# Optimization experiments

Hardware: AMD Instinct MI355X
Metric: run time of the kernel (lower is better)

The kernel has to match this reference:

```python
import jax, jax.numpy as jnp
import numpy as np

B_, S_, DM, DI, N_, R_, K_ = 2, 2048, 256, 512, 16, 32, 4
NB = 4  # 2 forward + 2 backward MambaBlocks


def setup_inputs() -> dict:
    key = jax.random.key(0)
    ks = jax.random.split(key, 16)
    def rn(k, shape, s=0.02):
        return jax.random.normal(k, shape, jnp.float32) * s
    A = jnp.log(jnp.arange(1, N_ + 1, dtype=jnp.float32))  # [N]
    return {
        'x': jax.random.normal(ks[0], (B_, S_, DM), jnp.float32),
        'in_w': rn(ks[1], (NB, DM, 2 * DI)),
        'conv_w': rn(ks[2], (NB, DI, K_), 0.3),
        'conv_b': jnp.zeros((NB, DI), jnp.float32),
        'A_log': jnp.broadcast_to(A, (NB, DI, N_)) + 0.0,
        'xd_w': rn(ks[3], (NB, DI, R_)),
        'xB_w': rn(ks[4], (NB, DI, N_)),
        'xC_w': rn(ks[5], (NB, DI, N_)),
        'dtp_w': rn(ks[6], (NB, R_, DI), R_ ** -0.5),
        'dtp_b': jax.random.uniform(ks[7], (NB, DI), jnp.float32,
                                    minval=jnp.log(0.001), maxval=jnp.log(0.1)),
        'D': jnp.ones((NB, DI), jnp.float32),
        'out_w': rn(ks[8], (NB, DI, DM)),
        'ln_g': jnp.ones((NB, DM), jnp.float32),
        'ln_b': jnp.zeros((NB, DM), jnp.float32),
        'merge_w': rn(ks[9], (2 * DM, DM)),
    }


def _layer_norm(x, g, b, eps=1e-5):
    m = jnp.mean(x, axis=-1, keepdims=True)
    v = jnp.mean(jnp.square(x - m), axis=-1, keepdims=True)
    return (x - m) * jax.lax.rsqrt(v + eps) * g + b


def _ssm_scan(dA, dBx, C):
    # dA, dBx: [B,S,DI,N]; C: [B,S,N] -> y: [B,S,DI]
    def step(h, inp):
        dA_t, dBx_t, C_t = inp
        h = dA_t * h + dBx_t                      # [B,DI,N]
        y = jnp.einsum('bdn,bn->bd', h, C_t)      # [B,DI]
        return h, y
    h0 = jnp.zeros(dA.shape[:1] + dA.shape[2:], dA.dtype)
    _, ys = jax.lax.scan(step, h0, (dA.transpose(1, 0, 2, 3),
                                    dBx.transpose(1, 0, 2, 3),
                                    C.transpose(1, 0, 2)))
    return ys.transpose(1, 0, 2)


def _mamba_block(x, in_w, conv_w, conv_b, A_log, xd_w, xB_w, xC_w,
                 dtp_w, dtp_b, D, out_w, g, b):
    res = x
    xn = _layer_norm(x, g, b)
    xz = xn @ in_w                                # [B,S,2*DI]
    xs, z = jnp.split(xz, 2, axis=-1)
    # causal depthwise conv: left pad K-1 (equals torch pad=K-1 then slice [:S])
    xc = jax.lax.conv_general_dilated(
        xs.transpose(0, 2, 1), conv_w[:, None, :], (1,), [(K_ - 1, 0)],
        dimension_numbers=('NCH', 'OIH', 'NCH'), feature_group_count=DI)
    xc = jax.nn.silu((xc + conv_b[None, :, None]).transpose(0, 2, 1))  # [B,S,DI]
    delta = jax.nn.softplus((xc @ xd_w) @ dtp_w + dtp_b)               # [B,S,DI]
    Bm = xc @ xB_w                                # [B,S,N]
    Cm = xc @ xC_w                                # [B,S,N]
    A = -jnp.exp(A_log)                           # [DI,N]
    dA = jnp.exp(delta[..., None] * A)            # [B,S,DI,N]
    dBx = (delta * xc)[..., None] * Bm[:, :, None, :]
    y = _ssm_scan(dA, dBx, Cm) + D * xc
    return (y * jax.nn.silu(z)) @ out_w + res


def reference(x, in_w, conv_w, conv_b, A_log, xd_w, xB_w, xC_w,
              dtp_w, dtp_b, D, out_w, ln_g, ln_b, merge_w):
    def blk(h, i):
        return _mamba_block(h, in_w[i], conv_w[i], conv_b[i], A_log[i],
                            xd_w[i], xB_w[i], xC_w[i], dtp_w[i], dtp_b[i],
                            D[i], out_w[i], ln_g[i], ln_b[i])
    fwd = blk(blk(x, 0), 1)
    bwd = blk(blk(x[:, ::-1], 2), 3)[:, ::-1]
    return jnp.concatenate([fwd, bwd], axis=-1) @ merge_w
```

## Files before the change

kernel.cpp:

```cpp
#include <hip/hip_runtime.h>

#define S_LEN 2048
#define DINNER 512
#define NCHUNK 64
#define CLEN 32

typedef unsigned short u16;
typedef short bf16x8 __attribute__((ext_vector_type(8)));
typedef unsigned short u16x8 __attribute__((ext_vector_type(8)));
typedef float f32x4 __attribute__((ext_vector_type(4)));

__device__ __forceinline__ float bf2f(u16 u) {
  unsigned int x = ((unsigned int)u) << 16;
  float f; __builtin_memcpy(&f, &x, 4); return f;
}
__device__ __forceinline__ u16 f2bf(float f) {
  unsigned int x; __builtin_memcpy(&x, &f, 4);
  return (u16)((x + 0x7FFFu + ((x >> 16) & 1u)) >> 16);
}
__device__ __forceinline__ float ldw(const void* p, size_t i, int isbf) {
  return isbf ? bf2f(((const u16*)p)[i]) : ((const float*)p)[i];
}
__device__ __forceinline__ float siluf(float x) { return x / (1.f + __expf(-x)); }
__device__ __forceinline__ float softplusf(float x) {
  if (x > 20.f) return x;
  return log1pf(__expf(x));
}

__global__ __launch_bounds__(256) void detect_kernel(const void* __restrict__ x,
                                                     int* __restrict__ flag) {
  __shared__ int cnt;
  if (threadIdx.x == 0) cnt = 0;
  __syncthreads();
  u16 u = ((const u16*)x)[2 * threadIdx.x];
  int e = (u >> 7) & 0xFF;
  if (e >= 0x60 && e <= 0x8F) atomicAdd(&cnt, 1);
  __syncthreads();
  if (threadIdx.x == 0) *flag = (cnt > 128) ? 1 : 0;
}

__global__ __launch_bounds__(256) void prep_kernel(
    const void* __restrict__ A_log,
    const void* __restrict__ in_w, const void* __restrict__ out_w,
    const void* __restrict__ merge_w,
    const void* __restrict__ xdw, const void* __restrict__ dtpw,
    const void* __restrict__ xBw, const void* __restrict__ xCw,
    const int* __restrict__ pf,
    float* __restrict__ Acp, u16* __restrict__ Wp_in, u16* __restrict__ Wp_out,
    u16* __restrict__ Wp_mg, u16* __restrict__ Wp_cmb)
{
  const int isbf = *pf;
  int b = blockIdx.x;
  int tid = threadIdx.x;
  __shared__ float smem[32 * 163];
  float* tile = smem;

  if (b < 128) {
    int idx = b * 256 + tid;
    Acp[idx] = -__expf(ldw(A_log, (size_t)idx, isbf));
    return;
  }
  b -= 128;

  if (b < 512 + 256 + 64) {
    const void* src; u16* dst; int K, N, nb64, kb, mat;
    if (b < 512)      { src = in_w;    dst = Wp_in;  K = 256; N = 1024;
                        nb64 = b % 16; kb = (b / 16) % 8; mat = b / 128; }
    else if (b < 768) { int c = b - 512; src = out_w; dst = Wp_out; K = 512; N = 256;
                        nb64 = c % 4; kb = (c / 4) % 16; mat = c / 64; }
    else              { int c = b - 768; src = merge_w; dst = Wp_mg; K = 512; N = 256;
                        nb64 = c % 4; kb = (c / 4) % 16; mat = 0; }
    size_t so = (size_t)mat * K * N;
    int kk = tid >> 3, nseg = (tid & 7) * 8;
#pragma unroll
    for (int j = 0; j < 8; ++j)
      tile[kk * 65 + nseg + j] =
          ldw(src, so + (size_t)(kb * 32 + kk) * N + nb64 * 64 + nseg + j, isbf);
    __syncthreads();
    int cc = tid >> 6, i0 = (tid & 63) * 8;
    int q = i0 >> 7, nn = (i0 >> 3) & 15;
    u16 outv[8];
#pragma unroll
    for (int j = 0; j < 8; ++j) outv[j] = f2bf(tile[(q * 8 + j) * 65 + cc * 16 + nn]);
    size_t doff = (size_t)mat * K * N + ((size_t)(nb64 * 4 + cc) * (K >> 5) + kb) * 512 + i0;
    *(u16x8*)(dst + doff) = *(const u16x8*)outv;
    return;
  }
  b -= 832;

  {
    int nb64 = b % 9, kb = (b / 9) % 16, mat = b / 144;
    float* xd = smem + 32 * 65;
    float* wt = smem + 32 * 98;
    if (nb64 < 8) {
      {
        int k = tid >> 3, j0 = (tid & 7) * 4;
#pragma unroll
        for (int j = 0; j < 4; ++j)
          xd[k * 33 + j0 + j] =
              ldw(xdw, (size_t)mat * 16384 + (size_t)(kb * 32 + k) * 32 + j0 + j, isbf);
        int jj = tid >> 3, n0l = (tid & 7) * 8;
#pragma unroll
        for (int n = 0; n < 8; ++n)
          wt[jj * 65 + n0l + n] =
              ldw(dtpw, (size_t)mat * 16384 + (size_t)jj * 512 + nb64 * 64 + n0l + n, isbf);
      }
      __syncthreads();
      for (int l = tid; l < 2048; l += 256) {
        int k = l >> 6, n = l & 63;
        float a = 0.f;
#pragma unroll
        for (int j = 0; j < 32; ++j) a += xd[k * 33 + j] * wt[j * 65 + n];
        tile[k * 65 + n] = a;
      }
    } else {
      for (int l = tid; l < 2048; l += 256) {
        int k = l >> 6, n = l & 63;
        int kg = kb * 32 + k;
        float v = 0.f;
        if (n < 16)      v = ldw(xBw, (size_t)mat * 8192 + (size_t)kg * 16 + n, isbf);
        else if (n < 32) v = ldw(xCw, (size_t)mat * 8192 + (size_t)kg * 16 + (n - 16), isbf);
        tile[k * 65 + n] = v;
      }
    }
    __syncthreads();
    int cc = tid >> 6, i0 = (tid & 63) * 8;
    int q = i0 >> 7, nn = (i0 >> 3) & 15;
    u16 outv[8];
#pragma unroll
    for (int j = 0; j < 8; ++j) outv[j] = f2bf(tile[(q * 8 + j) * 65 + cc * 16 + nn]);
    size_t doff = (size_t)mat * 294912 + ((size_t)(nb64 * 4 + cc) * 16 + kb) * 512 + i0;
    *(u16x8*)(Wp_cmb + doff) = *(const u16x8*)outv;
  }
}

__global__ __launch_bounds__(256) void ln_kernel(
    const void* __restrict__ x, const u16* __restrict__ obA, int it,
    const void* __restrict__ g, const void* __restrict__ bta,
    const int* __restrict__ pf, float* __restrict__ res, u16* __restrict__ xnb)
{
  const int isbf = *pf;
  int r = blockIdx.x;
  int tid = threadIdx.x;
  int chain = r >> 12, rr = r & 4095;
  int i = chain * 2 + it;
  size_t wo = (size_t)i * 256;
  float v;
  if (it == 0) {
    int b = rr >> 11, s = rr & 2047;
    int sr = chain ? (b * S_LEN + (S_LEN - 1 - s)) : rr;
    v = ldw(x, (size_t)sr * 256 + tid, isbf);
  } else {
    v = bf2f(obA[(size_t)r * 256 + tid]);
  }
  res[(size_t)r * 256 + tid] = v;
  float s1 = v, s2 = v * v;
#pragma unroll
  for (int o = 32; o > 0; o >>= 1) {
    s1 += __shfl_xor(s1, o, 64);
    s2 += __shfl_xor(s2, o, 64);
  }
  __shared__ float r1[4], r2[4];
  if ((tid & 63) == 0) { r1[tid >> 6] = s1; r2[tid >> 6] = s2; }
  __syncthreads();
  s1 = r1[0] + r1[1] + r1[2] + r1[3];
  s2 = r2[0] + r2[1] + r2[2] + r2[3];
  float mean = s1 * (1.f / 256.f);
  float var  = s2 * (1.f / 256.f) - mean * mean;
  float inv  = rsqrtf(var + 1e-5f);
  xnb[(size_t)r * 256 + tid] =
      f2bf((v - mean) * inv * ldw(g, wo + tid, isbf) + ldw(bta, wo + tid, isbf));
}

template<int OUTMODE>
__global__ __launch_bounds__(256) void gemm64(
    const u16* __restrict__ A, const u16* __restrict__ Wp, size_t woA, size_t woB, int mhalf,
    const float* __restrict__ res, void* __restrict__ Out, void* __restrict__ Out2,
    const void* __restrict__ bias, size_t boA, size_t boB,
    const int* __restrict__ pf, int N, int K, int nbx)
{
  const int isbf = *pf;
  __shared__ __align__(16) u16 Asb[2][4096];
  __shared__ __align__(16) u16 Bsb[2][4096];
  int tid = threadIdx.x;
  int gidx = blockIdx.x;
  int xcd = gidx & 7, rest = gidx >> 3;
  int nIdx = rest % nbx, mGrp = rest / nbx;
  int n0 = nIdx * 64, m0 = (xcd + (mGrp << 3)) * 64;
  size_t wo = (mhalf && m0 >= mhalf) ? woB : woA;
  int w = tid >> 6, lane = tid & 63;
  int q = lane >> 4, r = lane & 15;
  const int wm0 = (w >> 1) * 2, wn0 = (w & 1) * 2;
  const int kbs = K >> 5;
  f32x4 acc[2][2];
#pragma unroll
  for (int i = 0; i < 2; ++i)
#pragma unroll
    for (int j = 0; j < 2; ++j) acc[i][j] = (f32x4){0.f, 0.f, 0.f, 0.f};

  int sm = tid >> 2, sq = tid & 3;
  const u16* asrc = A + (size_t)(m0 + sm) * K + sq * 8;
  const int aoff = ((sm >> 4) * 4 + sq) * 128 + (sm & 15) * 8;
  int bnb = tid >> 6, binner = (tid & 63) * 8;
  const int boff = bnb * 512 + binner;
  const u16* bcol = Wp + wo + (size_t)((n0 >> 4) + bnb) * kbs * 512 + binner;

  u16x8 la0 = *(const u16x8*)(asrc);
  u16x8 la1 = *(const u16x8*)(asrc + 32);
  u16x8 lb0 = *(const u16x8*)(bcol);
  u16x8 lb1 = *(const u16x8*)(bcol + 512);

  int p = 0;
  for (int k0 = 0; k0 < K; k0 += 64, p ^= 1) {
    *(u16x8*)(Asb[p] + aoff)        = la0;
    *(u16x8*)(Asb[p] + aoff + 2048) = la1;
    *(u16x8*)(Bsb[p] + boff)        = lb0;
    *(u16x8*)(Bsb[p] + boff + 2048) = lb1;
    __syncthreads();
    if (k0 + 64 < K) {
      la0 = *(const u16x8*)(asrc + k0 + 64);
      la1 = *(const u16x8*)(asrc + k0 + 96);
      const u16* bs = bcol + (size_t)((k0 + 64) >> 5) * 512;
      lb0 = *(const u16x8*)bs;
      lb1 = *(const u16x8*)(bs + 512);
    }
#pragma unroll
    for (int ck = 0; ck < 2; ++ck) {
      const u16* Ab = Asb[p] + ck * 2048;
      const u16* Bb = Bsb[p] + ck * 2048;
      bf16x8 af[2], bfr[2];
#pragma unroll
      for (int i = 0; i < 2; ++i)
        af[i] = *(const bf16x8*)(Ab + ((wm0 + i) * 4 + q) * 128 + r * 8);
#pragma unroll
      for (int j = 0; j < 2; ++j)
        bfr[j] = *(const bf16x8*)(Bb + ((wn0 + j) * 4 + q) * 128 + r * 8);
#pragma unroll
      for (int i = 0; i < 2; ++i)
#pragma unroll
        for (int j = 0; j < 2; ++j)
          acc[i][j] = __builtin_amdgcn_mfma_f32_16x16x32_bf16(af[i], bfr[j], acc[i][j], 0, 0, 0);
    }
  }
#pragma unroll
  for (int i = 0; i < 2; ++i) {
    int rowb = m0 + (wm0 + i) * 16 + q * 4;
#pragma unroll
    for (int j = 0; j < 2; ++j) {
      int col = n0 + (wn0 + j) * 16 + r;
#pragma unroll
      for (int t = 0; t < 4; ++t) {
        int row = rowb + t;
        float v = acc[i][j][t];
        if (OUTMODE == 2 || OUTMODE == 3) { if (res) v += res[(size_t)row * N + col]; }
        if (OUTMODE == 1) {
          size_t lidx = (size_t)row * N + col;
          if (isbf) ((u16*)Out)[lidx] = f2bf(v); else ((float*)Out)[lidx] = v;
        } else if (OUTMODE == 2) {
          ((u16*)Out)[(size_t)row * N + col] = f2bf(v);
        } else if (OUTMODE == 3) {
          int orow, cofx;
          if (row < 4096) { orow = row; cofx = 0; }
          else {
            int rr = row - 4096; int bb = rr >> 11, ss = rr & 2047;
            orow = bb * S_LEN + (S_LEN - 1 - ss); cofx = 256;
          }
          ((u16*)Out)[(size_t)orow * 512 + col + cofx] = f2bf(v);
        } else if (OUTMODE == 5) {
          if (col < 512) {
            float bv = ldw(bias, ((row < 4096) ? boA : boB) + col, isbf);
            ((u16*)Out)[(size_t)row * 512 + col] = f2bf(softplusf(v + bv));
          } else if (col < 544) {
            ((float*)Out2)[(size_t)row * 32 + (col - 512)] = v;
          }
        }
      }
    }
  }
}

__global__ __launch_bounds__(256) void conv_kernel(
    const u16* __restrict__ xzb, const void* __restrict__ cw, const void* __restrict__ cb,
    int it, const int* __restrict__ pf, u16* __restrict__ xcb)
{
  const int isbf = *pf;
  int idx = blockIdx.x * 256 + threadIdx.x;
  int r = idx >> 6, dg = idx & 63;
  int d0 = dg << 3;
  int chain = r >> 12, rr = r & 4095;
  int i = chain * 2 + it;
  size_t ow = (size_t)i * 2048, ob = (size_t)i * 512;
  int s = rr & 2047;
  float acc[8];
#pragma unroll
  for (int j = 0; j < 8; ++j) acc[j] = ldw(cb, ob + d0 + j, isbf);
#pragma unroll
  for (int k = 0; k < 4; ++k) {
    int t = s - 3 + k;
    if (t >= 0) {
      u16x8 xv = *(const u16x8*)(xzb + (((size_t)(r + t - s)) << 10) + d0);
#pragma unroll
      for (int j = 0; j < 8; ++j)
        acc[j] += ldw(cw, ow + (size_t)(d0 + j) * 4 + k, isbf) * bf2f(xv[j]);
    }
  }
  u16 outv[8];
#pragma unroll
  for (int j = 0; j < 8; ++j) outv[j] = f2bf(siluf(acc[j]));
  *(u16x8*)(xcb + ((size_t)r << 9) + d0) = *(const u16x8*)outv;
}

__global__ __launch_bounds__(256) void scan_p1_kernel(
    const u16* __restrict__ xcb, const u16* __restrict__ delb, const float* __restrict__ dBC,
    const float* __restrict__ Acp, int it, const int* __restrict__ pf,
    float* __restrict__ aggA, float* __restrict__ aggB)
{
  __shared__ float sb[32][16];
  __shared__ u16 sdu[32][64];
  __shared__ u16 sxu[32][64];
  int tid = threadIdx.x;
  int di = tid >> 2, ng = tid & 3;
  int d0 = blockIdx.x << 6;
  int c = blockIdx.y, seq = blockIdx.z;
  int chain = seq >> 1, bb = seq & 1;
  int row0 = chain * 4096 + bb * S_LEN + c * CLEN;
  int i = chain * 2 + it;
  {
    int t = tid >> 3, e0 = (tid & 7) * 8;
    *(u16x8*)&sdu[t][e0] = *(const u16x8*)(delb + (size_t)(row0 + t) * 512 + d0 + e0);
    *(u16x8*)&sxu[t][e0] = *(const u16x8*)(xcb + (size_t)(row0 + t) * 512 + d0 + e0);
  }
  if (tid < 128) {
    int t = tid >> 2, e0 = (tid & 3) * 4;
    *(f32x4*)&sb[t][e0] = *(const f32x4*)(dBC + (size_t)(row0 + t) * 32 + e0);
  }
  f32x4 Ac = *(const f32x4*)(Acp + ((size_t)i * 512 + d0 + di) * 16 + ng * 4);
  __syncthreads();
  float h[4] = {0.f, 0.f, 0.f, 0.f};
  float ap[4] = {1.f, 1.f, 1.f, 1.f};
#pragma unroll 8
  for (int t = 0; t < CLEN; ++t) {
    float de = bf2f(sdu[t][di]);
    float dx = de * bf2f(sxu[t][di]);
    f32x4 B = *(const f32x4*)&sb[t][ng * 4];
#pragma unroll
    for (int j = 0; j < 4; ++j) {
      float e = __expf(de * Ac[j]);
      h[j] = e * h[j] + dx * B[j];
      ap[j] *= e;
    }
  }
  size_t o = (((size_t)(seq * NCHUNK + c) * DINNER) + d0 + di) * 16 + ng * 4;
  *(f32x4*)(aggA + o) = (f32x4){ap[0], ap[1], ap[2], ap[3]};
  *(f32x4*)(aggB + o) = (f32x4){h[0], h[1], h[2], h[3]};
}

__global__ __launch_bounds__(64) void scan_prefix_kernel(
    const float* __restrict__ aggA, float* __restrict__ aggB)
{
  int idx = blockIdx.x * 64 + threadIdx.x;
  int n = idx & 15, d = (idx >> 4) & 511, seq = idx >> 13;
  size_t o = (((size_t)(seq * NCHUNK) * DINNER) + d) * 16 + n;
  const size_t stride = (size_t)DINNER * 16;
  float h = 0.f;
  for (int c0 = 0; c0 < NCHUNK; c0 += 8) {
    float a[8], b[8];
#pragma unroll
    for (int j = 0; j < 8; ++j) {
      a[j] = aggA[o + (size_t)j * stride];
      b[j] = aggB[o + (size_t)j * stride];
    }
#pragma unroll
    for (int j = 0; j < 8; ++j) {
      aggB[o + (size_t)j * stride] = h;
      h = a[j] * h + b[j];
    }
    o += (size_t)8 * stride;
  }
}

__global__ __launch_bounds__(256) void scan_p3_kernel(
    const u16* __restrict__ xcb, const u16* __restrict__ delb, const float* __restrict__ dBC,
    const u16* __restrict__ xzb, const float* __restrict__ hpref,
    const float* __restrict__ Acp, const void* __restrict__ Dp,
    int it, const int* __restrict__ pf, u16* __restrict__ ymb)
{
  const int isbf = *pf;
  __shared__ float sbc[32][32];
  __shared__ float sy[32][64];
  __shared__ u16 sdu[32][64];
  __shared__ u16 sxu[32][64];
  __shared__ u16 szu[32][64];
  int tid = threadIdx.x;
  int di = tid >> 2, ng = tid & 3;
  int d0 = blockIdx.x << 6;
  int c = blockIdx.y, seq = blockIdx.z;
  int chain = seq >> 1, bb = seq & 1;
  int row0 = chain * 4096 + bb * S_LEN + c * CLEN;
  int i = chain * 2 + it;
  size_t oD = (size_t)i * 512;
  {
    int t = tid >> 3, e0 = (tid & 7) * 8;
    *(u16x8*)&sdu[t][e0] = *(const u16x8*)(delb + (size_t)(row0 + t) * 512 + d0 + e0);
    *(u16x8*)&sxu[t][e0] = *(const u16x8*)(xcb + (size_t)(row0 + t) * 512 + d0 + e0);
    *(u16x8*)&szu[t][e0] = *(const u16x8*)(xzb + ((size_t)(row0 + t) << 10) + 512 + d0 + e0);
  }
  {
    int t = tid >> 3, e0 = (tid & 7) * 4;
    *(f32x4*)&sbc[t][e0] = *(const f32x4*)(dBC + (size_t)(row0 + t) * 32 + e0);
  }
  f32x4 Ac = *(const f32x4*)(Acp + ((size_t)i * 512 + d0 + di) * 16 + ng * 4);
  float Dv = ldw(Dp, oD + d0 + di, isbf);
  float h[4];
  size_t o = (((size_t)(seq * NCHUNK + c) * DINNER) + d0 + di) * 16 + ng * 4;
  {
    f32x4 v = *(const f32x4*)(hpref + o);
    h[0] = v[0]; h[1] = v[1]; h[2] = v[2]; h[3] = v[3];
  }
  __syncthreads();
#pragma unroll 8
  for (int t = 0; t < CLEN; ++t) {
    float de = bf2f(sdu[t][di]);
    float xv = bf2f(sxu[t][di]);
    float dx = de * xv;
    f32x4 B = *(const f32x4*)&sbc[t][ng * 4];
    f32x4 C = *(const f32x4*)&sbc[t][16 + ng * 4];
    float yc = 0.f;
#pragma unroll
    for (int j = 0; j < 4; ++j) {
      float e = __expf(de * Ac[j]);
      h[j] = e * h[j] + dx * B[j];
      yc += h[j] * C[j];
    }
    yc += __shfl_xor(yc, 1, 64);
    yc += __shfl_xor(yc, 2, 64);
    if (ng == 0) sy[t][di] = yc + Dv * xv;
  }
  __syncthreads();
  int dcol = tid & 63;
#pragma unroll
  for (int k = 0; k < 8; ++k) {
    int t = (tid >> 6) + k * 4;
    float y = sy[t][dcol];
    float z = bf2f(szu[t][dcol]);
    ymb[(size_t)(row0 + t) * 512 + d0 + dcol] = f2bf(y * siluf(z));
  }
}

extern "C" void kernel_launch(void* const* d_in, const int* in_sizes, int n_in,
                              void* d_out, int out_size, void* d_ws, size_t ws_size,
                              hipStream_t stream)
{
  const void* x       = d_in[0];
  const void* in_w    = d_in[1];
  const void* conv_w  = d_in[2];
  const void* conv_b  = d_in[3];
  const void* A_log   = d_in[4];
  const void* xd_w    = d_in[5];
  const void* xB_w    = d_in[6];
  const void* xC_w    = d_in[7];
  const void* dtp_w   = d_in[8];
  const void* dtp_b   = d_in[9];
  const void* Dp      = d_in[10];
  const void* out_w   = d_in[11];
  const void* ln_g    = d_in[12];
  const void* ln_b    = d_in[13];
  const void* merge_w = d_in[14];

  float* ws    = (float*)d_ws;
  float* res   = ws;
  float* dBC   = res + (size_t)8192 * 256;
  float* aggA  = dBC + (size_t)8192 * 32;
  float* aggB  = aggA + (size_t)2097152;
  u16*   xz_bf = (u16*)(aggB + (size_t)2097152);
  u16*   xc_bf = xz_bf + (size_t)8192 * 1024;
  u16*   del_bf= xc_bf + (size_t)8192 * 512;
  u16*   Wp_in = del_bf + (size_t)8192 * 512;
  u16*   Wp_out= Wp_in + (size_t)4 * 262144;
  u16*   Wp_mg = Wp_out + (size_t)4 * 131072;
  u16*   Wp_cmb= Wp_mg + (size_t)131072;
  float* Acp   = (float*)(Wp_cmb + (size_t)4 * 294912);
  int*   flagp = (int*)(Acp + (size_t)4 * 8192);
  u16*   obA_bf= xz_bf;
  u16*   xn_bf = (u16*)aggA;
  u16*   ym_bf = (u16*)aggA;
  u16*   cat_bf= del_bf;

  dim3 blk(256);
  hipLaunchKernelGGL(detect_kernel, dim3(1), blk, 0, stream, x, flagp);
  hipLaunchKernelGGL(prep_kernel, dim3(1536), blk, 0, stream,
      A_log, in_w, out_w, merge_w, xd_w, dtp_w, xB_w, xC_w, flagp,
      Acp, Wp_in, Wp_out, Wp_mg, Wp_cmb);

  for (int it = 0; it < 2; ++it) {
    hipLaunchKernelGGL(ln_kernel, dim3(8192), blk, 0, stream,
        x, obA_bf, it, ln_g, ln_b, flagp, res, xn_bf);
    hipLaunchKernelGGL((gemm64<2>), dim3(16 * 128), blk, 0, stream,
        xn_bf, Wp_in, (size_t)it * 262144, (size_t)(2 + it) * 262144, 4096,
        (const float*)nullptr, (void*)xz_bf, (void*)nullptr,
        (const void*)nullptr, (size_t)0, (size_t)0, flagp, 1024, 256, 16);
    hipLaunchKernelGGL(conv_kernel, dim3(2048), blk, 0, stream,
        xz_bf, conv_w, conv_b, it, flagp, xc_bf);
    hipLaunchKernelGGL((gemm64<5>), dim3(9 * 128), blk, 0, stream,
        xc_bf, Wp_cmb, (size_t)it * 294912, (size_t)(2 + it) * 294912, 4096,
        (const float*)nullptr, (void*)del_bf, (void*)dBC,
        dtp_b, (size_t)it * 512, (size_t)(2 + it) * 512, flagp, 576, 512, 9);
    hipLaunchKernelGGL(scan_p1_kernel, dim3(8, NCHUNK, 4), blk, 0, stream,
        xc_bf, del_bf, dBC, Acp, it, flagp, aggA, aggB);
    hipLaunchKernelGGL(scan_prefix_kernel, dim3(512), dim3(64), 0, stream, aggA, aggB);
    hipLaunchKernelGGL(scan_p3_kernel, dim3(8, NCHUNK, 4), blk, 0, stream,
        xc_bf, del_bf, dBC, xz_bf, aggB, Acp, Dp, it, flagp, ym_bf);
    if (it == 0) {
      hipLaunchKernelGGL((gemm64<2>), dim3(4 * 128), blk, 0, stream,
          ym_bf, Wp_out, (size_t)0, (size_t)2 * 131072, 4096,
          res, (void*)obA_bf, (void*)nullptr,
          (const void*)nullptr, (size_t)0, (size_t)0, flagp, 256, 512, 4);
    } else {
      hipLaunchKernelGGL((gemm64<3>), dim3(4 * 128), blk, 0, stream,
          ym_bf, Wp_out, (size_t)1 * 131072, (size_t)3 * 131072, 4096,
          res, (void*)cat_bf, (void*)nullptr,
          (const void*)nullptr, (size_t)0, (size_t)0, flagp, 256, 512, 4);
    }
  }
  hipLaunchKernelGGL((gemm64<1>), dim3(4 * 64), blk, 0, stream,
      cat_bf, Wp_mg, (size_t)0, (size_t)0, 0,
      (const float*)nullptr, d_out, (void*)nullptr,
      (const void*)nullptr, (size_t)0, (size_t)0, flagp, 256, 512, 4);
}
```

Measured before the change: 404.3 us.

## Drop fp32 residual buffer, fuse detect into prep, vectorize layernorm

Removes the separate dtype-detect launch by computing the flag redundantly in every prep block. LayerNorm now processes one row per wavefront with 4-wide vector loads, avoiding shared-memory reduction and no longer writing an fp32 residual copy. The out-projection GEMM reads the residual directly from the input (it=0) or from a bf16 copy it writes alongside obA, saving residual traffic. The bf16 residual copy slightly changes numerics for the second block.

```diff
diff --git a/kernel.cpp b/kernel.cpp
--- a/kernel.cpp
+++ b/kernel.cpp
@@ -8,6 +8,7 @@
 typedef unsigned short u16;
 typedef short bf16x8 __attribute__((ext_vector_type(8)));
 typedef unsigned short u16x8 __attribute__((ext_vector_type(8)));
+typedef unsigned short u16x4 __attribute__((ext_vector_type(4)));
 typedef float f32x4 __attribute__((ext_vector_type(4)));
 
 __device__ __forceinline__ float bf2f(u16 u) {
@@ -27,31 +28,31 @@
   return log1pf(__expf(x));
 }
 
-__global__ __launch_bounds__(256) void detect_kernel(const void* __restrict__ x,
-                                                     int* __restrict__ flag) {
-  __shared__ int cnt;
-  if (threadIdx.x == 0) cnt = 0;
-  __syncthreads();
-  u16 u = ((const u16*)x)[2 * threadIdx.x];
-  int e = (u >> 7) & 0xFF;
-  if (e >= 0x60 && e <= 0x8F) atomicAdd(&cnt, 1);
-  __syncthreads();
-  if (threadIdx.x == 0) *flag = (cnt > 128) ? 1 : 0;
-}
-
 __global__ __launch_bounds__(256) void prep_kernel(
+    const void* __restrict__ xinp,
     const void* __restrict__ A_log,
     const void* __restrict__ in_w, const void* __restrict__ out_w,
     const void* __restrict__ merge_w,
     const void* __restrict__ xdw, const void* __restrict__ dtpw,
     const void* __restrict__ xBw, const void* __restrict__ xCw,
-    const int* __restrict__ pf,
+    int* __restrict__ flagp,
     float* __restrict__ Acp, u16* __restrict__ Wp_in, u16* __restrict__ Wp_out,
     u16* __restrict__ Wp_mg, u16* __restrict__ Wp_cmb)
 {
-  const int isbf = *pf;
   int b = blockIdx.x;
   int tid = threadIdx.x;
+  __shared__ int cnt_s;
+  if (tid == 0) cnt_s = 0;
+  __syncthreads();
+  {
+    u16 u = ((const u16*)xinp)[2 * tid];
+    int e = (u >> 7) & 0xFF;
+    if (e >= 0x60 && e <= 0x8F) atomicAdd(&cnt_s, 1);
+  }
+  __syncthreads();
+  const int isbf = (cnt_s > 128) ? 1 : 0;
+  if (b == 0 && tid == 0) *flagp = isbf;
+
   __shared__ float smem[32 * 163];
   float* tile = smem;
 
@@ -137,45 +138,55 @@
 __global__ __launch_bounds__(256) void ln_kernel(
     const void* __restrict__ x, const u16* __restrict__ obA, int it,
     const void* __restrict__ g, const void* __restrict__ bta,
-    const int* __restrict__ pf, float* __restrict__ res, u16* __restrict__ xnb)
+    const int* __restrict__ pf, u16* __restrict__ xnb)
 {
   const int isbf = *pf;
-  int r = blockIdx.x;
   int tid = threadIdx.x;
+  int w = tid >> 6, lane = tid & 63;
+  int r = blockIdx.x * 4 + w;
   int chain = r >> 12, rr = r & 4095;
   int i = chain * 2 + it;
   size_t wo = (size_t)i * 256;
-  float v;
+  int e0 = lane * 4;
+  float v[4];
   if (it == 0) {
     int b = rr >> 11, s = rr & 2047;
     int sr = chain ? (b * S_LEN + (S_LEN - 1 - s)) : rr;
-    v = ldw(x, (size_t)sr * 256 + tid, isbf);
+    if (isbf) {
+      u16x4 u = *(const u16x4*)((const u16*)x + (size_t)sr * 256 + e0);
+#pragma unroll
+      for (int j = 0; j < 4; ++j) v[j] = bf2f(u[j]);
+    } else {
+      f32x4 u = *(const f32x4*)((const float*)x + (size_t)sr * 256 + e0);
+#pragma unroll
+      for (int j = 0; j < 4; ++j) v[j] = u[j];
+    }
   } else {
-    v = bf2f(obA[(size_t)r * 256 + tid]);
-  }
-  res[(size_t)r * 256 + tid] = v;
-  float s1 = v, s2 = v * v;
+    u16x4 u = *(const u16x4*)(obA + (size_t)r * 256 + e0);
+#pragma unroll
+    for (int j = 0; j < 4; ++j) v[j] = bf2f(u[j]);
+  }
+  float s1 = v[0] + v[1] + v[2] + v[3];
+  float s2 = v[0] * v[0] + v[1] * v[1] + v[2] * v[2] + v[3] * v[3];
 #pragma unroll
   for (int o = 32; o > 0; o >>= 1) {
     s1 += __shfl_xor(s1, o, 64);
     s2 += __shfl_xor(s2, o, 64);
   }
-  __shared__ float r1[4], r2[4];
-  if ((tid & 63) == 0) { r1[tid >> 6] = s1; r2[tid >> 6] = s2; }
-  __syncthreads();
-  s1 = r1[0] + r1[1] + r1[2] + r1[3];
-  s2 = r2[0] + r2[1] + r2[2] + r2[3];
   float mean = s1 * (1.f / 256.f);
   float var  = s2 * (1.f / 256.f) - mean * mean;
   float inv  = rsqrtf(var + 1e-5f);
-  xnb[(size_t)r * 256 + tid] =
-      f2bf((v - mean) * inv * ldw(g, wo + tid, isbf) + ldw(bta, wo + tid, isbf));
-}
-
-template<int OUTMODE>
+  u16 o4[4];
+#pragma unroll
+  for (int j = 0; j < 4; ++j)
+    o4[j] = f2bf((v[j] - mean) * inv * ldw(g, wo + e0 + j, isbf) + ldw(bta, wo + e0 + j, isbf));
+  *(u16x4*)(xnb + (size_t)r * 256 + e0) = *(const u16x4*)o4;
+}
+
+template<int OUTMODE, int RESMODE>
 __global__ __launch_bounds__(256) void gemm64(
     const u16* __restrict__ A, const u16* __restrict__ Wp, size_t woA, size_t woB, int mhalf,
-    const float* __restrict__ res, void* __restrict__ Out, void* __restrict__ Out2,
+    const void* __restrict__ resv, void* __restrict__ Out, void* __restrict__ Out2,
     const void* __restrict__ bias, size_t boA, size_t boB,
     const int* __restrict__ pf, int N, int K, int nbx)
 {
@@ -252,12 +263,23 @@
       for (int t = 0; t < 4; ++t) {
         int row = rowb + t;
         float v = acc[i][j][t];
-        if (OUTMODE == 2 || OUTMODE == 3) { if (res) v += res[(size_t)row * N + col]; }
+        if (OUTMODE == 2 || OUTMODE == 3) {
+          if (RESMODE == 1) {
+            int rr2 = row & 4095, ch = row >> 12;
+            int bb = rr2 >> 11, ss = rr2 & 2047;
+            int sr = ch ? (bb * S_LEN + (S_LEN - 1 - ss)) : rr2;
+            v += ldw(resv, (size_t)sr * 256 + col, isbf);
+          } else if (RESMODE == 2) {
+            v += bf2f(((const u16*)resv)[(size_t)row * 256 + col]);
+          }
+        }
         if (OUTMODE == 1) {
           size_t lidx = (size_t)row * N + col;
           if (isbf) ((u16*)Out)[lidx] = f2bf(v); else ((float*)Out)[lidx] = v;
         } else if (OUTMODE == 2) {
-          ((u16*)Out)[(size_t)row * N + col] = f2bf(v);
+          u16 ov = f2bf(v);
+          ((u16*)Out)[(size_t)row * N + col] = ov;
+          if (Out2) ((u16*)Out2)[(size_t)row * N + col] = ov;
         } else if (OUTMODE == 3) {
           int orow, cofx;
           if (row < 4096) { orow = row; cofx = 0; }
@@ -468,8 +490,8 @@
   const void* merge_w = d_in[14];
 
   float* ws    = (float*)d_ws;
-  float* res   = ws;
-  float* dBC   = res + (size_t)8192 * 256;
+  u16*   res_bf= (u16*)ws;
+  float* dBC   = ws + (size_t)8192 * 256;
   float* aggA  = dBC + (size_t)8192 * 32;
   float* aggB  = aggA + (size_t)2097152;
   u16*   xz_bf = (u16*)(aggB + (size_t)2097152);
@@ -487,23 +509,22 @@
   u16*   cat_bf= del_bf;
 
   dim3 blk(256);
-  hipLaunchKernelGGL(detect_kernel, dim3(1), blk, 0, stream, x, flagp);
   hipLaunchKernelGGL(prep_kernel, dim3(1536), blk, 0, stream,
-      A_log, in_w, out_w, merge_w, xd_w, dtp_w, xB_w, xC_w, flagp,
+      x, A_log, in_w, out_w, merge_w, xd_w, dtp_w, xB_w, xC_w, flagp,
       Acp, Wp_in, Wp_out, Wp_mg, Wp_cmb);
 
   for (int it = 0; it < 2; ++it) {
-    hipLaunchKernelGGL(ln_kernel, dim3(8192), blk, 0, stream,
-        x, obA_bf, it, ln_g, ln_b, flagp, res, xn_bf);
-    hipLaunchKernelGGL((gemm64<2>), dim3(16 * 128), blk, 0, stream,
+    hipLaunchKernelGGL(ln_kernel, dim3(2048), blk, 0, stream,
+        x, obA_bf, it, ln_g, ln_b, flagp, xn_bf);
+    hipLaunchKernelGGL((gemm64<2, 0>), dim3(16 * 128), blk, 0, stream,
         xn_bf, Wp_in, (size_t)it * 262144, (size_t)(2 + it) * 262144, 4096,
-        (const float*)nullptr, (void*)xz_bf, (void*)nullptr,
+        (const void*)nullptr, (void*)xz_bf, (void*)nullptr,
         (const void*)nullptr, (size_t)0, (size_t)0, flagp, 1024, 256, 16);
     hipLaunchKernelGGL(conv_kernel, dim3(2048), blk, 0, stream,
         xz_bf, conv_w, conv_b, it, flagp, xc_bf);
-    hipLaunchKernelGGL((gemm64<5>), dim3(9 * 128), blk, 0, stream,
+    hipLaunchKernelGGL((gemm64<5, 0>), dim3(9 * 128), blk, 0, stream,
         xc_bf, Wp_cmb, (size_t)it * 294912, (size_t)(2 + it) * 294912, 4096,
-        (const float*)nullptr, (void*)del_bf, (void*)dBC,
+        (const void*)nullptr, (void*)del_bf, (void*)dBC,
         dtp_b, (size_t)it * 512, (size_t)(2 + it) * 512, flagp, 576, 512, 9);
     hipLaunchKernelGGL(scan_p1_kernel, dim3(8, NCHUNK, 4), blk, 0, stream,
         xc_bf, del_bf, dBC, Acp, it, flagp, aggA, aggB);
@@ -511,19 +532,19 @@
     hipLaunchKernelGGL(scan_p3_kernel, dim3(8, NCHUNK, 4), blk, 0, stream,
         xc_bf, del_bf, dBC, xz_bf, aggB, Acp, Dp, it, flagp, ym_bf);
     if (it == 0) {
-      hipLaunchKernelGGL((gemm64<2>), dim3(4 * 128), blk, 0, stream,
+      hipLaunchKernelGGL((gemm64<2, 1>), dim3(4 * 128), blk, 0, stream,
           ym_bf, Wp_out, (size_t)0, (size_t)2 * 131072, 4096,
-          res, (void*)obA_bf, (void*)nullptr,
+          x, (void*)obA_bf, (void*)res_bf,
           (const void*)nullptr, (size_t)0, (size_t)0, flagp, 256, 512, 4);
     } else {
-      hipLaunchKernelGGL((gemm64<3>), dim3(4 * 128), blk, 0, stream,
+      hipLaunchKernelGGL((gemm64<3, 2>), dim3(4 * 128), blk, 0, stream,
           ym_bf, Wp_out, (size_t)1 * 131072, (size_t)3 * 131072, 4096,
-          res, (void*)cat_bf, (void*)nullptr,
+          (const void*)res_bf, (void*)cat_bf, (void*)nullptr,
           (const void*)nullptr, (size_t)0, (size_t)0, flagp, 256, 512, 4);
     }
   }
-  hipLaunchKernelGGL((gemm64<1>), dim3(4 * 64), blk, 0, stream,
+  hipLaunchKernelGGL((gemm64<1, 0>), dim3(4 * 64), blk, 0, stream,
       cat_bf, Wp_mg, (size_t)0, (size_t)0, 0,
-      (const float*)nullptr, d_out, (void*)nullptr,
+      (const void*)nullptr, d_out, (void*)nullptr,
       (const void*)nullptr, (size_t)0, (size_t)0, flagp, 256, 512, 4);
 }
```

Result: faster. 392.8 us (-2.9%).
